# Optimization experiments

Measured on AMD Instinct MI355X. Metric: run time of the kernel, lower is better.

The kernel has to match this reference:

```python
import jax, jax.numpy as jnp
import numpy as np

B, H, W = 32, 64, 64
D = 8        # input_dim (capsule dim of incoming caps)
C = 8        # input_ch (number of incoming capsule types)
DIM = 8      # dim_capsule (output capsule dim)
NCH = 8      # n_channels (number of output capsule types)


def _gconv(x, w, groups, stride=1):
    # x: NHWC, w: HWIO with I = in_ch/groups, O = total out (grouped by output blocks)
    return jax.lax.conv_general_dilated(
        x, w, (stride, stride), 'SAME',
        dimension_numbers=('NHWC', 'HWIO', 'NHWC'),
        feature_group_count=groups)


def setup_inputs():
    key = jax.random.key(0)
    ks = jax.random.split(key, 5)
    inputs = jax.random.normal(ks[0], (B, H, W, D, C), jnp.float32)
    Att_W = jax.random.normal(ks[1], (1, 1, DIM, C, C * NCH), jnp.float32) * 0.05
    ConvTrans_W = jax.random.normal(ks[2], (3, 3, D, C * DIM * NCH), jnp.float32) * 0.05
    ConvTrans_B = jnp.zeros((C * DIM * NCH,), jnp.float32)
    FeaExt_W = jax.random.normal(ks[3], (3, 3, DIM, DIM * NCH), jnp.float32) * 0.05
    FeaExt_B = jnp.zeros((DIM * NCH,), jnp.float32)
    CapsAct_W = jax.random.normal(ks[4], (1, 1, DIM, DIM * NCH), jnp.float32) * 0.05
    CapsAct_B = jnp.zeros((DIM * NCH,), jnp.float32)
    return {'inputs': inputs, 'Att_W': Att_W, 'ConvTrans_W': ConvTrans_W,
            'ConvTrans_B': ConvTrans_B, 'FeaExt_W': FeaExt_W, 'FeaExt_B': FeaExt_B,
            'CapsAct_W': CapsAct_W, 'CapsAct_B': CapsAct_B}


def reference(inputs, Att_W, ConvTrans_W, ConvTrans_B, FeaExt_W, FeaExt_B,
              CapsAct_W, CapsAct_B):
    # --- ConvTrans: per input-capsule-type 3x3 conv (== grouped conv over C groups) ---
    # inputs [B,H,W,D,C] -> [B,H,W,C*D] with group-major ordering
    xt = jnp.transpose(inputs, (0, 1, 2, 4, 3)).reshape(B, H, W, C * D)
    # ConvTrans_W [3,3,D, C*DIM*NCH]: output block i is the kernel for input group i
    y = _gconv(xt, ConvTrans_W, groups=C) + ConvTrans_B  # [B,H,W, C*DIM*NCH]
    # -> u[b,h,w,d,c_in,n]  (matches concat+transpose in the original)
    u = y.reshape(B, H, W, C, DIM, NCH).transpose(0, 1, 2, 4, 3, 5)

    # --- Attention: conv3d with kernel [1,1,DIM,C,C] per output type n (VALID over DIM) ---
    # Att_W [1,1,DIM,C,C*NCH] -> A[d, c_in, n, c_out]
    A = Att_W[0, 0].reshape(DIM, C, NCH, C)
    att = jnp.einsum('bhwdcn,dcno->bhwon', u, A)       # [B,H,W,C,NCH]
    att = jax.nn.softmax(att, axis=3)                  # softmax over input_ch
    v = jnp.einsum('bhwdon,bhwon->bhwdn', u, att)      # weighted sum over input_ch

    # --- FeaExt (3x3, grouped over NCH) + ReLU, then CapsAct (1x1, grouped) ---
    vt = jnp.transpose(v, (0, 1, 2, 4, 3)).reshape(B, H, W, NCH * DIM)
    h1 = jax.nn.relu(_gconv(vt, FeaExt_W, groups=NCH) + FeaExt_B)
    h2 = _gconv(h1, CapsAct_W, groups=NCH) + CapsAct_B
    out = h2.reshape(B, H, W, NCH, DIM).transpose(0, 1, 2, 4, 3)  # [B,H,W,DIM,NCH]
    return out
```

## Files before the change

kernel.cpp:

```cpp
#include <hip/hip_runtime.h>

#define HH 64
#define WW 64

typedef _Float16 f16;
typedef f16 f16x8 __attribute__((ext_vector_type(8)));
typedef f16 f16x4 __attribute__((ext_vector_type(4)));
typedef float f32x4 __attribute__((ext_vector_type(4)));

#define M1_H 0
#define BU_H 49152
#define BF_H 98304
#define BC_H 110592
#define VT_H 114688
#define PREP_N (64 + 114688)

__global__ __launch_bounds__(256) void prep_kernel(
    const float* __restrict__ attw, const float* __restrict__ ctw,
    const float* __restrict__ ctb, const float* __restrict__ few,
    const float* __restrict__ caw, float* __restrict__ ws) {
  int i = blockIdx.x * 256 + threadIdx.x;
  if (i >= PREP_N) return;
  f16* hb = (f16*)(ws + 64);
  if (i < 64) {
    int s = i >> 4, l15 = i & 15;
    int o = 2 * s + (l15 >> 3), n = l15 & 7;
    float acc = 0.f;
    for (int c = 0; c < 8; ++c)
      for (int d = 0; d < 8; ++d)
        acc += ctb[c * 64 + d * 8 + n] * attw[d * 512 + c * 64 + n * 8 + o];
    ws[i] = acc;
    return;
  }
  int z = i - 64;
  if (z < BU_H) {
    int j = z & 7, lane = (z >> 3) & 63, rest = z >> 9;
    int rs = rest % 12, c = rest / 12;
    int r = rs >> 2, s = rs & 3;
    int q = lane >> 4, l15 = lane & 15;
    int t = r * 4 + q;
    int o = 2 * s + (l15 >> 3), n = l15 & 7;
    float acc = 0.f;
    if (t < 9)
      for (int d = 0; d < 8; ++d)
        acc += ctw[(t * 8 + j) * 512 + c * 64 + d * 8 + n] *
               attw[d * 512 + c * 64 + n * 8 + o];
    hb[M1_H + z] = (f16)acc;
  } else if (z < BF_H) {
    int z2 = z - BU_H;
    int j = z2 & 7, lane = (z2 >> 3) & 63, rest = z2 >> 9;
    int rs = rest % 12, c = rest / 12;
    int r = rs >> 2, s = rs & 3;
    int q = lane >> 4, l15 = lane & 15;
    int t = r * 4 + q;
    int d = 2 * s + (l15 >> 3), n = l15 & 7;
    float v = (t < 9) ? ctw[(t * 8 + j) * 512 + c * 64 + d * 8 + n] : 0.f;
    hb[z] = (f16)v;
  } else if (z < BC_H) {
    int z2 = z - BF_H;
    int j = z2 & 7, lane = (z2 >> 3) & 63, rest = z2 >> 9;
    int r = rest % 3, g = rest / 3;
    int q = lane >> 4, l15 = lane & 15;
    int t = r * 4 + q;
    int d = 2 * (j & 3) + (j >> 2);
    float v = 0.f;
    if (t < 9 && ((l15 >> 3) == (g & 1)))
      v = few[(t * 8 + d) * 64 + g * 8 + (l15 & 7)];
    hb[z] = (f16)v;
  } else if (z < VT_H) {
    int z2 = z - BC_H;
    int j = z2 & 7, lane = (z2 >> 3) & 63, rest = z2 >> 9;
    int s = rest & 3, c2 = rest >> 2;
    int q = lane >> 4, l15 = lane & 15;
    int nk = c2 * 4 + q;
    int nc = 2 * s + (l15 >> 3);
    float v = (nk == nc) ? caw[j * 64 + nc * 8 + (l15 & 7)] : 0.f;
    hb[z] = (f16)v;
  }
}

__global__ __launch_bounds__(256, 2) void caps_stage1(
    const float* __restrict__ in, const float* __restrict__ ws,
    const float* __restrict__ ctb, f16* __restrict__ vt) {
  __shared__ f16 xt[181 * 72];
  __shared__ f16 attb[128 * 72];
  int bid = blockIdx.x;
  int b = bid >> 5, t5 = bid & 31;
  int ty = t5 >> 3, tx = t5 & 7;
  int tid = threadIdx.x;

  for (int i = tid; i < 181 * 8; i += 256) {
    int c = i & 7, hp = i >> 3;
    float xs[8] = {0.f, 0.f, 0.f, 0.f, 0.f, 0.f, 0.f, 0.f};
    if (hp < 180) {
      int hy = hp / 10, hx = hp - hy * 10;
      int gy = ty * 16 + hy - 1, gx = tx * 8 + hx - 1;
      if (gy >= 0 && gy < HH && gx >= 0 && gx < WW) {
        const float* src = in + (((b * HH + gy) * WW + gx) * 64 + c);
#pragma unroll
        for (int d = 0; d < 8; ++d) xs[d] = src[d * 8];
      }
    }
    f16x8 pk;
#pragma unroll
    for (int d = 0; d < 8; ++d) pk[d] = (f16)xs[d];
    *(f16x8*)&xt[hp * 72 + c * 8] = pk;
  }
  __syncthreads();

  int w = __builtin_amdgcn_readfirstlane(tid >> 6);
  int lane = tid & 63;
  int q = lane >> 4, l15 = lane & 15;
  int h = l15 >> 3, n = l15 & 7;

  int hpt[2][3];
#pragma unroll
  for (int i2 = 0; i2 < 2; ++i2) {
    int pyA = (2 * w + i2) * 2 + h;
    int pxA = l15 & 7;
#pragma unroll
    for (int r = 0; r < 3; ++r) {
      int t = r * 4 + q;
      int hp = 180;
      if (t < 9) {
        int ky = t / 3, kx = t - ky * 3;
        hp = (pyA + ky) * 10 + pxA + kx;
      }
      hpt[i2][r] = hp * 72;
    }
  }

  const f16x8* m1v = (const f16x8*)((const f16*)(ws + 64) + M1_H);
  const f16x8* buv = (const f16x8*)((const f16*)(ws + 64) + BU_H);
  const float* lb = ws;

  f32x4 L[2][4];
#pragma unroll
  for (int s = 0; s < 4; ++s) {
    float v0 = lb[s * 16 + l15];
    L[0][s] = (f32x4){v0, v0, v0, v0};
    L[1][s] = (f32x4){v0, v0, v0, v0};
  }
#pragma unroll 1
  for (int c = 0; c < 8; ++c) {
    f16x8 bm[12];
#pragma unroll
    for (int rs = 0; rs < 12; ++rs) bm[rs] = m1v[(c * 12 + rs) * 64 + lane];
    f16x8 a[2][3];
#pragma unroll
    for (int i2 = 0; i2 < 2; ++i2)
#pragma unroll
      for (int r = 0; r < 3; ++r)
        a[i2][r] = *(const f16x8*)&xt[hpt[i2][r] + c * 8];
#pragma unroll
    for (int i2 = 0; i2 < 2; ++i2)
#pragma unroll
      for (int s = 0; s < 4; ++s)
#pragma unroll
        for (int r = 0; r < 3; ++r)
          L[i2][s] = __builtin_amdgcn_mfma_f32_16x16x32_f16(
              a[i2][r], bm[r * 4 + s], L[i2][s], 0, 0, 0);
  }

#pragma unroll
  for (int i2 = 0; i2 < 2; ++i2) {
    int pbase = (2 * w + i2) * 16 + q * 4;
#pragma unroll
    for (int r = 0; r < 4; ++r) {
      float v0 = L[i2][0][r], v1 = L[i2][1][r], v2 = L[i2][2][r], v3 = L[i2][3][r];
      float pm = fmaxf(fmaxf(v0, v1), fmaxf(v2, v3));
      float m = fmaxf(pm, __shfl_xor(pm, 8));
      float e0 = __expf(v0 - m), e1 = __expf(v1 - m);
      float e2 = __expf(v2 - m), e3 = __expf(v3 - m);
      float ps = e0 + e1 + e2 + e3;
      float inv = 1.f / (ps + __shfl_xor(ps, 8));
      int ab = (pbase + r) * 72 + n * 8 + h;
      attb[ab + 0] = (f16)(e0 * inv);
      attb[ab + 2] = (f16)(e1 * inv);
      attb[ab + 4] = (f16)(e2 * inv);
      attb[ab + 6] = (f16)(e3 * inv);
    }
  }
  __syncthreads();

  f16x8 atp[2][4];
#pragma unroll
  for (int i2 = 0; i2 < 2; ++i2)
#pragma unroll
    for (int r = 0; r < 4; ++r)
      atp[i2][r] = *(const f16x8*)&attb[((2 * w + i2) * 16 + q * 4 + r) * 72 + n * 8];

  f32x4 V[2][4];
#pragma unroll
  for (int s = 0; s < 4; ++s) {
    V[0][s] = (f32x4){0.f, 0.f, 0.f, 0.f};
    V[1][s] = (f32x4){0.f, 0.f, 0.f, 0.f};
  }
#pragma unroll 1
  for (int c = 0; c < 8; ++c) {
    f16x8 bu[12];
#pragma unroll
    for (int rs = 0; rs < 12; ++rs) bu[rs] = buv[(c * 12 + rs) * 64 + lane];
    f16x8 a[2][3];
#pragma unroll
    for (int i2 = 0; i2 < 2; ++i2)
#pragma unroll
      for (int r = 0; r < 3; ++r)
        a[i2][r] = *(const f16x8*)&xt[hpt[i2][r] + c * 8];
    f32x4 U[2][4];
#pragma unroll
    for (int s = 0; s < 4; ++s) {
      float bv = ctb[c * 64 + s * 16 + l15];
      U[0][s] = (f32x4){bv, bv, bv, bv};
      U[1][s] = (f32x4){bv, bv, bv, bv};
    }
#pragma unroll
    for (int i2 = 0; i2 < 2; ++i2)
#pragma unroll
      for (int s = 0; s < 4; ++s)
#pragma unroll
        for (int r = 0; r < 3; ++r)
          U[i2][s] = __builtin_amdgcn_mfma_f32_16x16x32_f16(
              a[i2][r], bu[r * 4 + s], U[i2][s], 0, 0, 0);
#pragma unroll
    for (int i2 = 0; i2 < 2; ++i2)
#pragma unroll
      for (int r = 0; r < 4; ++r) {
        float af = (float)atp[i2][r][c];
#pragma unroll
        for (int s = 0; s < 4; ++s) V[i2][s][r] += U[i2][s][r] * af;
      }
  }

  __syncthreads();
  f16* vtmp = attb;
#pragma unroll
  for (int i2 = 0; i2 < 2; ++i2)
#pragma unroll
    for (int r = 0; r < 4; ++r) {
      int p = (2 * w + i2) * 16 + q * 4 + r;
      f16x4 st;
#pragma unroll
      for (int s = 0; s < 4; ++s) st[s] = (f16)V[i2][s][r];
      *(f16x4*)&vtmp[p * 72 + n * 8 + h * 4] = st;
    }
  __syncthreads();
  for (int idx = tid; idx < 1024; idx += 256) {
    int p = idx >> 3, q2 = idx & 7;
    float4 val = *(float4*)&vtmp[p * 72 + q2 * 8];
    int gy = ty * 16 + (p >> 3), gx = tx * 8 + (p & 7);
    ((float4*)(vt + ((b * HH + gy) * WW + gx) * 64))[q2] = val;
  }
}

__global__ __launch_bounds__(256, 2) void caps_stage2(
    const f16* __restrict__ vt, const float* __restrict__ ws,
    const float* __restrict__ fb, const float* __restrict__ cab,
    float* __restrict__ out) {
  __shared__ float smemf[8704];
  f16* vtile = (f16*)smemf;
  int bid = blockIdx.x;
  int b = bid >> 5, t5 = bid & 31;
  int ty = t5 >> 3, tx = t5 & 7;
  int tid = threadIdx.x;

  for (int i = tid; i < 181 * 8; i += 256) {
    int q2 = i & 7, hp = i >> 3;
    float4 val = make_float4(0.f, 0.f, 0.f, 0.f);
    if (hp < 180) {
      int hy = hp / 10, hx = hp - hy * 10;
      int gy = ty * 16 + hy - 1, gx = tx * 8 + hx - 1;
      if (gy >= 0 && gy < HH && gx >= 0 && gx < WW)
        val = ((const float4*)(vt + ((b * HH + gy) * WW + gx) * 64))[q2];
    }
    *(float4*)&vtile[hp * 72 + q2 * 8] = val;
  }
  __syncthreads();

  int w = __builtin_amdgcn_readfirstlane(tid >> 6);
  int lane = tid & 63;
  int q = lane >> 4, l15 = lane & 15;
  int h = l15 >> 3, j7 = l15 & 7;

  int hpt[2][3];
#pragma unroll
  for (int i2 = 0; i2 < 2; ++i2) {
    int pyA = (2 * w + i2) * 2 + h;
#pragma unroll
    for (int r = 0; r < 3; ++r) {
      int t = r * 4 + q;
      int hp = 180;
      if (t < 9) {
        int ky = t / 3, kx = t - ky * 3;
        hp = (pyA + ky) * 10 + j7 + kx;
      }
      hpt[i2][r] = hp * 72;
    }
  }

  const f16x8* bfv = (const f16x8*)((const f16*)(ws + 64) + BF_H);
  const f16x8* bcv = (const f16x8*)((const f16*)(ws + 64) + BC_H);

  f32x4 L[2][4];
#pragma unroll
  for (int s = 0; s < 4; ++s) {
    float bvv = fb[(2 * s + h) * 8 + j7];
    L[0][s] = (f32x4){bvv, bvv, bvv, bvv};
    L[1][s] = (f32x4){bvv, bvv, bvv, bvv};
  }
#pragma unroll
  for (int g = 0; g < 8; ++g) {
    int sg = g >> 1;
#pragma unroll
    for (int r = 0; r < 3; ++r) {
      f16x8 bf = bfv[(g * 3 + r) * 64 + lane];
#pragma unroll
      for (int i2 = 0; i2 < 2; ++i2) {
        f16x8 a = *(const f16x8*)&vtile[hpt[i2][r] + g * 8];
        L[i2][sg] = __builtin_amdgcn_mfma_f32_16x16x32_f16(a, bf, L[i2][sg], 0, 0, 0);
      }
    }
  }
#pragma unroll
  for (int i2 = 0; i2 < 2; ++i2)
#pragma unroll
    for (int s = 0; s < 4; ++s)
#pragma unroll
      for (int r = 0; r < 4; ++r) L[i2][s][r] = fmaxf(L[i2][s][r], 0.f);

  __syncthreads();
  f16* h1t = (f16*)smemf;
#pragma unroll
  for (int i2 = 0; i2 < 2; ++i2)
#pragma unroll
    for (int s = 0; s < 4; ++s)
#pragma unroll
      for (int r = 0; r < 4; ++r)
        h1t[((2 * w + i2) * 16 + q * 4 + r) * 72 + (2 * s + h) * 8 + j7] =
            (f16)L[i2][s][r];
  __syncthreads();

  f32x4 H[2][4];
#pragma unroll
  for (int s = 0; s < 4; ++s) {
    float bvv = cab[(2 * s + h) * 8 + j7];
    H[0][s] = (f32x4){bvv, bvv, bvv, bvv};
    H[1][s] = (f32x4){bvv, bvv, bvv, bvv};
  }
#pragma unroll
  for (int c2 = 0; c2 < 2; ++c2) {
    f16x8 a2[2];
#pragma unroll
    for (int i2 = 0; i2 < 2; ++i2)
      a2[i2] = *(const f16x8*)&h1t[((2 * w + i2) * 16 + l15) * 72 + c2 * 32 + q * 8];
#pragma unroll
    for (int s = 0; s < 4; ++s) {
      f16x8 bc = bcv[(c2 * 4 + s) * 64 + lane];
#pragma unroll
      for (int i2 = 0; i2 < 2; ++i2)
        H[i2][s] = __builtin_amdgcn_mfma_f32_16x16x32_f16(a2[i2], bc, H[i2][s], 0, 0, 0);
    }
  }

  __syncthreads();
  float* outbuf = smemf;
#pragma unroll
  for (int i2 = 0; i2 < 2; ++i2)
#pragma unroll
    for (int s = 0; s < 4; ++s)
#pragma unroll
      for (int r = 0; r < 4; ++r)
        outbuf[((2 * w + i2) * 16 + q * 4 + r) * 68 + j7 * 8 + 2 * s + h] =
            H[i2][s][r];
  __syncthreads();

  for (int idx = tid; idx < 2048; idx += 256) {
    int p = idx >> 4, q4 = idx & 15;
    float4 val = *(float4*)&outbuf[p * 68 + q4 * 4];
    int gy = ty * 16 + (p >> 3), gx = tx * 8 + (p & 7);
    *(float4*)(out + ((b * HH + gy) * WW + gx) * 64 + q4 * 4) = val;
  }
}

extern "C" void kernel_launch(void* const* d_in, const int* in_sizes, int n_in,
                              void* d_out, int out_size, void* d_ws, size_t ws_size,
                              hipStream_t stream) {
  const float* inputs = (const float*)d_in[0];
  const float* attw   = (const float*)d_in[1];
  const float* ctw    = (const float*)d_in[2];
  const float* ctb    = (const float*)d_in[3];
  const float* few    = (const float*)d_in[4];
  const float* fb     = (const float*)d_in[5];
  const float* caw    = (const float*)d_in[6];
  const float* cab    = (const float*)d_in[7];
  float* out = (float*)d_out;
  float* ws  = (float*)d_ws;
  f16* vt = (f16*)(ws + 64) + VT_H;

  prep_kernel<<<(PREP_N + 255) / 256, 256, 0, stream>>>(attw, ctw, ctb, few, caw, ws);
  caps_stage1<<<32 * 32, 256, 0, stream>>>(inputs, ws, ctb, vt);
  caps_stage2<<<32 * 32, 256, 0, stream>>>(vt, ws, fb, cab, out);
}
```

Baseline: 149.0 us.

## Double-buffer weight fragment loads in stage1 loops and unroll the input staging

Both channel loops in caps_stage1 now use ping-pong register buffers. The weight fragments and bias for the next channel are loaded while the MFMAs for the current channel run, which hides global-load latency. Stage 2 now reads attention weights from LDS per channel instead of holding them in registers. It also processes one i2 half at a time to limit live U registers. The input staging loop is fully unrolled. Doubling the weight registers raises VGPR pressure, which may hurt occupancy at launch bounds of 2 blocks.

Result: faster. 141.2 us (-5.3%).

```diff
diff --git a/kernel.cpp b/kernel.cpp
--- a/kernel.cpp
+++ b/kernel.cpp
@@ -89,22 +89,26 @@
   int ty = t5 >> 3, tx = t5 & 7;
   int tid = threadIdx.x;
 
-  for (int i = tid; i < 181 * 8; i += 256) {
-    int c = i & 7, hp = i >> 3;
-    float xs[8] = {0.f, 0.f, 0.f, 0.f, 0.f, 0.f, 0.f, 0.f};
-    if (hp < 180) {
-      int hy = hp / 10, hx = hp - hy * 10;
-      int gy = ty * 16 + hy - 1, gx = tx * 8 + hx - 1;
-      if (gy >= 0 && gy < HH && gx >= 0 && gx < WW) {
-        const float* src = in + (((b * HH + gy) * WW + gx) * 64 + c);
-#pragma unroll
-        for (int d = 0; d < 8; ++d) xs[d] = src[d * 8];
+#pragma unroll
+  for (int k = 0; k < 6; ++k) {
+    int i = tid + k * 256;
+    if (i < 181 * 8) {
+      int c = i & 7, hp = i >> 3;
+      float xs[8] = {0.f, 0.f, 0.f, 0.f, 0.f, 0.f, 0.f, 0.f};
+      if (hp < 180) {
+        int hy = hp / 10, hx = hp - hy * 10;
+        int gy = ty * 16 + hy - 1, gx = tx * 8 + hx - 1;
+        if (gy >= 0 && gy < HH && gx >= 0 && gx < WW) {
+          const float* src = in + (((b * HH + gy) * WW + gx) * 64 + c);
+#pragma unroll
+          for (int d = 0; d < 8; ++d) xs[d] = src[d * 8];
+        }
       }
-    }
-    f16x8 pk;
-#pragma unroll
-    for (int d = 0; d < 8; ++d) pk[d] = (f16)xs[d];
-    *(f16x8*)&xt[hp * 72 + c * 8] = pk;
+      f16x8 pk;
+#pragma unroll
+      for (int d = 0; d < 8; ++d) pk[d] = (f16)xs[d];
+      *(f16x8*)&xt[hp * 72 + c * 8] = pk;
+    }
   }
   __syncthreads();
 
@@ -141,11 +145,12 @@
     L[0][s] = (f32x4){v0, v0, v0, v0};
     L[1][s] = (f32x4){v0, v0, v0, v0};
   }
-#pragma unroll 1
-  for (int c = 0; c < 8; ++c) {
-    f16x8 bm[12];
-#pragma unroll
-    for (int rs = 0; rs < 12; ++rs) bm[rs] = m1v[(c * 12 + rs) * 64 + lane];
+
+  f16x8 bmA[12], bmB[12];
+#pragma unroll
+  for (int rs = 0; rs < 12; ++rs) bmA[rs] = m1v[rs * 64 + lane];
+
+  auto p1step = [&](int c, const f16x8(&bm)[12]) {
     f16x8 a[2][3];
 #pragma unroll
     for (int i2 = 0; i2 < 2; ++i2)
@@ -160,7 +165,29 @@
         for (int r = 0; r < 3; ++r)
           L[i2][s] = __builtin_amdgcn_mfma_f32_16x16x32_f16(
               a[i2][r], bm[r * 4 + s], L[i2][s], 0, 0, 0);
-  }
+  };
+
+#pragma unroll 1
+  for (int cc = 0; cc < 4; ++cc) {
+    int c0 = 2 * cc;
+#pragma unroll
+    for (int rs = 0; rs < 12; ++rs)
+      bmB[rs] = m1v[((c0 + 1) * 12 + rs) * 64 + lane];
+    p1step(c0, bmA);
+    if (cc < 3) {
+#pragma unroll
+      for (int rs = 0; rs < 12; ++rs)
+        bmA[rs] = m1v[((c0 + 2) * 12 + rs) * 64 + lane];
+    }
+    p1step(c0 + 1, bmB);
+  }
+
+  f16x8 buA[12], buB[12];
+#pragma unroll
+  for (int rs = 0; rs < 12; ++rs) buA[rs] = buv[rs * 64 + lane];
+  float cbA[4], cbB[4];
+#pragma unroll
+  for (int s = 0; s < 4; ++s) cbA[s] = ctb[s * 16 + l15];
 
 #pragma unroll
   for (int i2 = 0; i2 < 2; ++i2) {
@@ -183,12 +210,12 @@
   }
   __syncthreads();
 
-  f16x8 atp[2][4];
+  int ab[2][4];
 #pragma unroll
   for (int i2 = 0; i2 < 2; ++i2)
 #pragma unroll
     for (int r = 0; r < 4; ++r)
-      atp[i2][r] = *(const f16x8*)&attb[((2 * w + i2) * 16 + q * 4 + r) * 72 + n * 8];
+      ab[i2][r] = ((2 * w + i2) * 16 + q * 4 + r) * 72 + n * 8;
 
   f32x4 V[2][4];
 #pragma unroll
@@ -196,40 +223,49 @@
     V[0][s] = (f32x4){0.f, 0.f, 0.f, 0.f};
     V[1][s] = (f32x4){0.f, 0.f, 0.f, 0.f};
   }
+
+  auto p2step = [&](int c, const f16x8(&bu)[12], const float(&cb)[4]) {
+#pragma unroll
+    for (int i2 = 0; i2 < 2; ++i2) {
+      f16x8 a[3];
+#pragma unroll
+      for (int r = 0; r < 3; ++r)
+        a[r] = *(const f16x8*)&xt[hpt[i2][r] + c * 8];
+      f32x4 U[4];
+#pragma unroll
+      for (int s = 0; s < 4; ++s) U[s] = (f32x4){cb[s], cb[s], cb[s], cb[s]};
+#pragma unroll
+      for (int s = 0; s < 4; ++s)
+#pragma unroll
+        for (int r = 0; r < 3; ++r)
+          U[s] = __builtin_amdgcn_mfma_f32_16x16x32_f16(
+              a[r], bu[r * 4 + s], U[s], 0, 0, 0);
+#pragma unroll
+      for (int r = 0; r < 4; ++r) {
+        float af = (float)attb[ab[i2][r] + c];
+#pragma unroll
+        for (int s = 0; s < 4; ++s) V[i2][s][r] += U[s][r] * af;
+      }
+    }
+  };
+
 #pragma unroll 1
-  for (int c = 0; c < 8; ++c) {
-    f16x8 bu[12];
-#pragma unroll
-    for (int rs = 0; rs < 12; ++rs) bu[rs] = buv[(c * 12 + rs) * 64 + lane];
-    f16x8 a[2][3];
-#pragma unroll
-    for (int i2 = 0; i2 < 2; ++i2)
-#pragma unroll
-      for (int r = 0; r < 3; ++r)
-        a[i2][r] = *(const f16x8*)&xt[hpt[i2][r] + c * 8];
-    f32x4 U[2][4];
-#pragma unroll
-    for (int s = 0; s < 4; ++s) {
-      float bv = ctb[c * 64 + s * 16 + l15];
-      U[0][s] = (f32x4){bv, bv, bv, bv};
-      U[1][s] = (f32x4){bv, bv, bv, bv};
-    }
-#pragma unroll
-    for (int i2 = 0; i2 < 2; ++i2)
-#pragma unroll
-      for (int s = 0; s < 4; ++s)
-#pragma unroll
-        for (int r = 0; r < 3; ++r)
-          U[i2][s] = __builtin_amdgcn_mfma_f32_16x16x32_f16(
-              a[i2][r], bu[r * 4 + s], U[i2][s], 0, 0, 0);
-#pragma unroll
-    for (int i2 = 0; i2 < 2; ++i2)
-#pragma unroll
-      for (int r = 0; r < 4; ++r) {
-        float af = (float)atp[i2][r][c];
-#pragma unroll
-        for (int s = 0; s < 4; ++s) V[i2][s][r] += U[i2][s][r] * af;
-      }
+  for (int cc = 0; cc < 4; ++cc) {
+    int c0 = 2 * cc;
+#pragma unroll
+    for (int rs = 0; rs < 12; ++rs)
+      buB[rs] = buv[((c0 + 1) * 12 + rs) * 64 + lane];
+#pragma unroll
+    for (int s = 0; s < 4; ++s) cbB[s] = ctb[(c0 + 1) * 64 + s * 16 + l15];
+    p2step(c0, buA, cbA);
+    if (cc < 3) {
+#pragma unroll
+      for (int rs = 0; rs < 12; ++rs)
+        buA[rs] = buv[((c0 + 2) * 12 + rs) * 64 + lane];
+#pragma unroll
+      for (int s = 0; s < 4; ++s) cbA[s] = ctb[(c0 + 2) * 64 + s * 16 + l15];
+    }
+    p2step(c0 + 1, buB, cbB);
   }
 
   __syncthreads();
```

## Stage MFMA weight fragments through double-buffered LDS via async global_load_lds

Applied to the files above, without the earlier changes.

Stage 1 no longer has each wave load its own copy of the 12 B-fragments per channel from global memory. The weight matrices are now streamed into a shared double buffer with global_load_lds, one fragment row at a time, prefetched two steps ahead and overlapped with the input tile load and the MFMAs. The attention weights are read from LDS on the fly and the bias is added after accumulation. Stage 2 hoists its CapsAct weight fragments into registers before the tile load. The cost is a barrier after every one of the 48 k-steps, which adds synchronisation and may limit overlap, plus higher register use in stage 2.

Measured after the change: 148.1 us. Within noise of the previous version (-0.7%).

```diff
diff --git a/kernel.cpp b/kernel.cpp
--- a/kernel.cpp
+++ b/kernel.cpp
@@ -7,6 +7,9 @@
 typedef f16 f16x8 __attribute__((ext_vector_type(8)));
 typedef f16 f16x4 __attribute__((ext_vector_type(4)));
 typedef float f32x4 __attribute__((ext_vector_type(4)));
+
+typedef __attribute__((address_space(3))) void lds_void;
+typedef __attribute__((address_space(1))) const void gbl_void;
 
 #define M1_H 0
 #define BU_H 49152
@@ -84,34 +87,51 @@
     const float* __restrict__ ctb, f16* __restrict__ vt) {
   __shared__ f16 xt[181 * 72];
   __shared__ f16 attb[128 * 72];
+  __shared__ f16 bstage[2][2048];
   int bid = blockIdx.x;
   int b = bid >> 5, t5 = bid & 31;
   int ty = t5 >> 3, tx = t5 & 7;
   int tid = threadIdx.x;
-
-  for (int i = tid; i < 181 * 8; i += 256) {
-    int c = i & 7, hp = i >> 3;
-    float xs[8] = {0.f, 0.f, 0.f, 0.f, 0.f, 0.f, 0.f, 0.f};
-    if (hp < 180) {
-      int hy = hp / 10, hx = hp - hy * 10;
-      int gy = ty * 16 + hy - 1, gx = tx * 8 + hx - 1;
-      if (gy >= 0 && gy < HH && gx >= 0 && gx < WW) {
-        const float* src = in + (((b * HH + gy) * WW + gx) * 64 + c);
-#pragma unroll
-        for (int d = 0; d < 8; ++d) xs[d] = src[d * 8];
-      }
-    }
-    f16x8 pk;
-#pragma unroll
-    for (int d = 0; d < 8; ++d) pk[d] = (f16)xs[d];
-    *(f16x8*)&xt[hp * 72 + c * 8] = pk;
-  }
-  __syncthreads();
-
   int w = __builtin_amdgcn_readfirstlane(tid >> 6);
   int lane = tid & 63;
   int q = lane >> 4, l15 = lane & 15;
   int h = l15 >> 3, n = l15 & 7;
+
+  const f16* hb = (const f16*)(ws + 64);
+  const f16* m1h = hb + M1_H;
+  const f16* buh = hb + BU_H;
+  const float* lb = ws;
+
+  auto stage = [&](const f16* src, int k, int bufi) {
+    __builtin_amdgcn_global_load_lds(
+        (gbl_void*)(src + (4 * k + w) * 512 + lane * 8),
+        (lds_void*)&bstage[bufi][w * 512], 16, 0, 0);
+  };
+
+  stage(m1h, 0, 0);
+  stage(m1h, 1, 1);
+
+#pragma unroll
+  for (int k = 0; k < 6; ++k) {
+    int i = tid + k * 256;
+    if (i < 181 * 8) {
+      int c = i & 7, hp = i >> 3;
+      float xs[8] = {0.f, 0.f, 0.f, 0.f, 0.f, 0.f, 0.f, 0.f};
+      if (hp < 180) {
+        int hy = hp / 10, hx = hp - hy * 10;
+        int gy = ty * 16 + hy - 1, gx = tx * 8 + hx - 1;
+        if (gy >= 0 && gy < HH && gx >= 0 && gx < WW) {
+          const float* src = in + (((b * HH + gy) * WW + gx) * 64 + c);
+#pragma unroll
+          for (int d = 0; d < 8; ++d) xs[d] = src[d * 8];
+        }
+      }
+      f16x8 pk;
+#pragma unroll
+      for (int d = 0; d < 8; ++d) pk[d] = (f16)xs[d];
+      *(f16x8*)&xt[hp * 72 + c * 8] = pk;
+    }
+  }
 
   int hpt[2][3];
 #pragma unroll
@@ -130,10 +150,6 @@
     }
   }
 
-  const f16x8* m1v = (const f16x8*)((const f16*)(ws + 64) + M1_H);
-  const f16x8* buv = (const f16x8*)((const f16*)(ws + 64) + BU_H);
-  const float* lb = ws;
-
   f32x4 L[2][4];
 #pragma unroll
   for (int s = 0; s < 4; ++s) {
@@ -141,25 +157,30 @@
     L[0][s] = (f32x4){v0, v0, v0, v0};
     L[1][s] = (f32x4){v0, v0, v0, v0};
   }
+  __syncthreads();
+
 #pragma unroll 1
-  for (int c = 0; c < 8; ++c) {
-    f16x8 bm[12];
-#pragma unroll
-    for (int rs = 0; rs < 12; ++rs) bm[rs] = m1v[(c * 12 + rs) * 64 + lane];
-    f16x8 a[2][3];
-#pragma unroll
-    for (int i2 = 0; i2 < 2; ++i2)
-#pragma unroll
-      for (int r = 0; r < 3; ++r)
-        a[i2][r] = *(const f16x8*)&xt[hpt[i2][r] + c * 8];
-#pragma unroll
-    for (int i2 = 0; i2 < 2; ++i2)
+  for (int cc = 0; cc < 8; ++cc) {
+#pragma unroll
+    for (int r = 0; r < 3; ++r) {
+      int k = cc * 3 + r;
+      int bufi = k & 1;
+      f16x8 bm[4];
 #pragma unroll
       for (int s = 0; s < 4; ++s)
-#pragma unroll
-        for (int r = 0; r < 3; ++r)
-          L[i2][s] = __builtin_amdgcn_mfma_f32_16x16x32_f16(
-              a[i2][r], bm[r * 4 + s], L[i2][s], 0, 0, 0);
+        bm[s] = *(const f16x8*)&bstage[bufi][s * 512 + lane * 8];
+      f16x8 a0 = *(const f16x8*)&xt[hpt[0][r] + cc * 8];
+      f16x8 a1 = *(const f16x8*)&xt[hpt[1][r] + cc * 8];
+#pragma unroll
+      for (int s = 0; s < 4; ++s) {
+        L[0][s] = __builtin_amdgcn_mfma_f32_16x16x32_f16(a0, bm[s], L[0][s], 0, 0, 0);
+        L[1][s] = __builtin_amdgcn_mfma_f32_16x16x32_f16(a1, bm[s], L[1][s], 0, 0, 0);
+      }
+      __syncthreads();
+      int k2 = k + 2;
+      if (k2 < 24) stage(m1h, k2, bufi);
+      else stage(buh, k2 - 24, bufi);
+    }
   }
 
 #pragma unroll
@@ -183,12 +204,12 @@
   }
   __syncthreads();
 
-  f16x8 atp[2][4];
+  int ab[2][4];
 #pragma unroll
   for (int i2 = 0; i2 < 2; ++i2)
 #pragma unroll
     for (int r = 0; r < 4; ++r)
-      atp[i2][r] = *(const f16x8*)&attb[((2 * w + i2) * 16 + q * 4 + r) * 72 + n * 8];
+      ab[i2][r] = ((2 * w + i2) * 16 + q * 4 + r) * 72 + n * 8;
 
   f32x4 V[2][4];
 #pragma unroll
@@ -196,43 +217,47 @@
     V[0][s] = (f32x4){0.f, 0.f, 0.f, 0.f};
     V[1][s] = (f32x4){0.f, 0.f, 0.f, 0.f};
   }
+
 #pragma unroll 1
-  for (int c = 0; c < 8; ++c) {
-    f16x8 bu[12];
-#pragma unroll
-    for (int rs = 0; rs < 12; ++rs) bu[rs] = buv[(c * 12 + rs) * 64 + lane];
-    f16x8 a[2][3];
+  for (int cc = 0; cc < 8; ++cc) {
+    float cb[4];
+#pragma unroll
+    for (int s = 0; s < 4; ++s) cb[s] = ctb[cc * 64 + s * 16 + l15];
+    f32x4 U[2][4];
 #pragma unroll
     for (int i2 = 0; i2 < 2; ++i2)
 #pragma unroll
-      for (int r = 0; r < 3; ++r)
-        a[i2][r] = *(const f16x8*)&xt[hpt[i2][r] + c * 8];
-    f32x4 U[2][4];
-#pragma unroll
-    for (int s = 0; s < 4; ++s) {
-      float bv = ctb[c * 64 + s * 16 + l15];
-      U[0][s] = (f32x4){bv, bv, bv, bv};
-      U[1][s] = (f32x4){bv, bv, bv, bv};
+      for (int s = 0; s < 4; ++s) U[i2][s] = (f32x4){0.f, 0.f, 0.f, 0.f};
+#pragma unroll
+    for (int r = 0; r < 3; ++r) {
+      int k = cc * 3 + r;
+      int bufi = k & 1;
+      f16x8 bm[4];
+#pragma unroll
+      for (int s = 0; s < 4; ++s)
+        bm[s] = *(const f16x8*)&bstage[bufi][s * 512 + lane * 8];
+      f16x8 a0 = *(const f16x8*)&xt[hpt[0][r] + cc * 8];
+      f16x8 a1 = *(const f16x8*)&xt[hpt[1][r] + cc * 8];
+#pragma unroll
+      for (int s = 0; s < 4; ++s) {
+        U[0][s] = __builtin_amdgcn_mfma_f32_16x16x32_f16(a0, bm[s], U[0][s], 0, 0, 0);
+        U[1][s] = __builtin_amdgcn_mfma_f32_16x16x32_f16(a1, bm[s], U[1][s], 0, 0, 0);
+      }
+      __syncthreads();
+      int k2 = k + 2;
+      if (k2 < 24) stage(buh, k2, bufi);
     }
 #pragma unroll
     for (int i2 = 0; i2 < 2; ++i2)
 #pragma unroll
-      for (int s = 0; s < 4; ++s)
-#pragma unroll
-        for (int r = 0; r < 3; ++r)
-          U[i2][s] = __builtin_amdgcn_mfma_f32_16x16x32_f16(
-              a[i2][r], bu[r * 4 + s], U[i2][s], 0, 0, 0);
-#pragma unroll
-    for (int i2 = 0; i2 < 2; ++i2)
-#pragma unroll
-      for (int r = 0; r < 4; ++r) {
-        float af = (float)atp[i2][r][c];
-#pragma unroll
-        for (int s = 0; s < 4; ++s) V[i2][s][r] += U[i2][s][r] * af;
-      }
-  }
-
-  __syncthreads();
+      for (int r4 = 0; r4 < 4; ++r4) {
+        float af = (float)attb[ab[i2][r4] + cc];
+#pragma unroll
+        for (int s = 0; s < 4; ++s)
+          V[i2][s][r4] += (U[i2][s][r4] + cb[s]) * af;
+      }
+  }
+
   f16* vtmp = attb;
 #pragma unroll
   for (int i2 = 0; i2 < 2; ++i2)
@@ -263,6 +288,15 @@
   int b = bid >> 5, t5 = bid & 31;
   int ty = t5 >> 3, tx = t5 & 7;
   int tid = threadIdx.x;
+  int w = __builtin_amdgcn_readfirstlane(tid >> 6);
+  int lane = tid & 63;
+
+  const f16x8* bfv = (const f16x8*)((const f16*)(ws + 64) + BF_H);
+  const f16x8* bcv = (const f16x8*)((const f16*)(ws + 64) + BC_H);
+
+  f16x8 bcf[8];
+#pragma unroll
+  for (int k = 0; k < 8; ++k) bcf[k] = bcv[k * 64 + lane];
 
   for (int i = tid; i < 181 * 8; i += 256) {
     int q2 = i & 7, hp = i >> 3;
@@ -277,8 +311,6 @@
   }
   __syncthreads();
 
-  int w = __builtin_amdgcn_readfirstlane(tid >> 6);
-  int lane = tid & 63;
   int q = lane >> 4, l15 = lane & 15;
   int h = l15 >> 3, j7 = l15 & 7;
 
@@ -298,9 +330,6 @@
     }
   }
 
-  const f16x8* bfv = (const f16x8*)((const f16*)(ws + 64) + BF_H);
-  const f16x8* bcv = (const f16x8*)((const f16*)(ws + 64) + BC_H);
-
   f32x4 L[2][4];
 #pragma unroll
   for (int s = 0; s < 4; ++s) {
@@ -355,10 +384,10 @@
       a2[i2] = *(const f16x8*)&h1t[((2 * w + i2) * 16 + l15) * 72 + c2 * 32 + q * 8];
 #pragma unroll
     for (int s = 0; s < 4; ++s) {
-      f16x8 bc = bcv[(c2 * 4 + s) * 64 + lane];
 #pragma unroll
       for (int i2 = 0; i2 < 2; ++i2)
-        H[i2][s] = __builtin_amdgcn_mfma_f32_16x16x32_f16(a2[i2], bc, H[i2][s], 0, 0, 0);
+        H[i2][s] = __builtin_amdgcn_mfma_f32_16x16x32_f16(
+            a2[i2], bcf[c2 * 4 + s], H[i2][s], 0, 0, 0);
     }
   }
 
```
